# Kernel optimization log

Hardware: AMD Instinct MI355X
Metric: run time of the kernel (lower is better)

Reference implementation:

```python
import jax, jax.numpy as jnp
import numpy as np

N_NODES = 50000
N_EDGES = 640000
D_IN = 128
D_H1 = 128
D_H2 = 256
NEG_SLOPE = 0.2


def setup_inputs() -> dict:
    key = jax.random.key(0)
    ks = jax.random.split(key, 12)
    s = 1.0 / np.sqrt(D_IN)
    inp = {
        'x': jax.random.normal(ks[0], (N_NODES, D_IN), dtype=jnp.float32),
        'edge_index': jax.random.randint(ks[1], (2, N_EDGES), 0, N_NODES, dtype=jnp.int64),
        # GATv2 layer 1: 128 -> 128 (separate lin_l / lin_r, attention vec, residual proj, bias)
        'Wl1': jax.random.normal(ks[2], (D_IN, D_H1), dtype=jnp.float32) * s,
        'Wr1': jax.random.normal(ks[3], (D_IN, D_H1), dtype=jnp.float32) * s,
        'att1': jax.random.normal(ks[4], (D_H1,), dtype=jnp.float32) * s,
        'Wres1': jax.random.normal(ks[5], (D_IN, D_H1), dtype=jnp.float32) * s,
        'b1': jnp.zeros((D_H1,), dtype=jnp.float32),
        # GATv2 layer 2: 128 -> 256
        'Wl2': jax.random.normal(ks[6], (D_H1, D_H2), dtype=jnp.float32) * s,
        'Wr2': jax.random.normal(ks[7], (D_H1, D_H2), dtype=jnp.float32) * s,
        'att2': jax.random.normal(ks[8], (D_H2,), dtype=jnp.float32) * s,
        'Wres2': jax.random.normal(ks[9], (D_H1, D_H2), dtype=jnp.float32) * s,
        'b2': jnp.zeros((D_H2,), dtype=jnp.float32),
    }
    return inp


def _gatv2_layer(x, Wl, Wr, att, Wres, b, src, dst, n_nodes):
    """GATv2Conv (heads=1, residual=True, eval mode/no dropout).
    score e_ij = att . LeakyReLU(Wl x_src + Wr x_dst); softmax over incoming edges per dst;
    out_dst = sum_j alpha_ij * (Wl x_src) + residual + bias.
    """
    xl = x @ Wl                      # [N, F]
    xr = x @ Wr                      # [N, F]
    h = xl[src] + xr[dst]            # [E, F]  gather (irregular access)
    e = jax.nn.leaky_relu(h, NEG_SLOPE) @ att   # [E]
    # segment softmax over destination nodes
    m = jax.ops.segment_max(e, dst, num_segments=n_nodes)      # [N]
    w = jnp.exp(e - m[dst])                                     # [E]
    denom = jax.ops.segment_sum(w, dst, num_segments=n_nodes)   # [N]
    alpha = w / (denom[dst] + 1e-16)                             # [E]
    out = jax.ops.segment_sum(alpha[:, None] * xl[src], dst, num_segments=n_nodes)  # [N, F]
    return out + x @ Wres + b


def reference(x, edge_index, Wl1, Wr1, att1, Wres1, b1, Wl2, Wr2, att2, Wres2, b2):
    src = edge_index[0]
    dst = edge_index[1]
    h = _gatv2_layer(x, Wl1, Wr1, att1, Wres1, b1, src, dst, N_NODES)
    h = jax.nn.elu(h)
    out = _gatv2_layer(h, Wl2, Wr2, att2, Wres2, b2, src, dst, N_NODES)
    return out
```

## Files before the change

kernel.cpp:

```cpp
#include <hip/hip_runtime.h>

typedef unsigned short u16;
typedef unsigned int u32;
typedef __attribute__((ext_vector_type(8))) short bf16x8;
typedef __attribute__((ext_vector_type(4))) float f32x4;

#define NN 50000
#define NE 640000

__device__ __forceinline__ float bfl(u32 u) { return __uint_as_float(u << 16); }
__device__ __forceinline__ float bfh(u32 u) { return __uint_as_float(u & 0xffff0000u); }
__device__ __forceinline__ float bf1(u16 v) { return __uint_as_float(((u32)v) << 16); }
__device__ __forceinline__ u16 f2bf(float f) {
  u32 u = __float_as_uint(f);
  u32 r = (u + 0x7fffu + ((u >> 16) & 1u)) >> 16;
  return (u16)r;
}

__global__ void probe_kernel(const u16* __restrict__ x, const int* __restrict__ ei,
                             int* __restrict__ flags) {
  __shared__ int s_f32, s_i32;
  if (threadIdx.x == 0) { s_f32 = 0; s_i32 = 0; }
  __syncthreads();
  int lf = 0, li = 0;
  for (int i = threadIdx.x; i < 8192; i += 256) {
    float v = bf1(x[i]);
    if (!(fabsf(v) < 1e8f)) lf = 1;
    if (ei[2 * i + 1] != 0) li = 1;
  }
  if (lf) s_f32 = 1;
  if (li) s_i32 = 1;
  __syncthreads();
  if (threadIdx.x == 0) {
    flags[0] = s_f32;
    flags[1] = s_i32 ? 0 : 1;
  }
}

__device__ __forceinline__ int edge_val(const int* __restrict__ w, long j, int i64) {
  return i64 ? w[2 * j] : w[j];
}

__global__ void count_kernel(const int* __restrict__ ei, const int* __restrict__ flags,
                             int* __restrict__ cnt, int E) {
  int e = blockIdx.x * blockDim.x + threadIdx.x;
  if (e >= E) return;
  int d = edge_val(ei, (long)E + e, flags[1]);
  if ((u32)d < (u32)NN) atomicAdd(&cnt[d], 1);
}

__global__ void scan_local(const int* __restrict__ cnt, int* __restrict__ excl,
                           int* __restrict__ bsum, int n) {
  __shared__ int sd[256];
  int t = threadIdx.x;
  int g = blockIdx.x * 256 + t;
  int v = (g < n) ? cnt[g] : 0;
  sd[t] = v;
  __syncthreads();
  for (int off = 1; off < 256; off <<= 1) {
    int x = (t >= off) ? sd[t - off] : 0;
    __syncthreads();
    sd[t] += x;
    __syncthreads();
  }
  int incl = sd[t];
  if (g < n) excl[g] = incl - v;
  if (t == 255) bsum[blockIdx.x] = incl;
}

__global__ void scan_totals(const int* __restrict__ bsum, int* __restrict__ boff, int nb) {
  __shared__ int sd[256];
  int t = threadIdx.x;
  int v = (t < nb) ? bsum[t] : 0;
  sd[t] = v;
  __syncthreads();
  for (int off = 1; off < 256; off <<= 1) {
    int x = (t >= off) ? sd[t - off] : 0;
    __syncthreads();
    sd[t] += x;
    __syncthreads();
  }
  if (t < nb) boff[t] = sd[t] - v;
}

__global__ void scan_add(const int* __restrict__ excl, const int* __restrict__ boff,
                         const int* __restrict__ cnt, int* __restrict__ rowptr,
                         int* __restrict__ fillp, int n) {
  int g = blockIdx.x * 256 + threadIdx.x;
  if (g < n) {
    int e2 = excl[g] + boff[blockIdx.x];
    rowptr[g] = e2;
    fillp[g] = e2;
    if (g == n - 1) rowptr[n] = e2 + cnt[g];
  }
}

__global__ void fill_kernel(const int* __restrict__ ei, const int* __restrict__ flags,
                            int* __restrict__ fillp, int* __restrict__ col, int E) {
  int e = blockIdx.x * blockDim.x + threadIdx.x;
  if (e >= E) return;
  int i64 = flags[1];
  int s = edge_val(ei, (long)e, i64);
  int d = edge_val(ei, (long)E + e, i64);
  if ((u32)d >= (u32)NN) return;
  int p = atomicAdd(&fillp[d], 1);
  col[p] = ((u32)s < (u32)NN) ? s : 0;
}

__global__ void transpose_w(const void* W0, const void* W1, const void* W2,
                            const void* W3, const void* W4, const void* W5,
                            u16* T0, u16* T1, u16* T2, u16* T3, u16* T4, u16* T5,
                            const int* __restrict__ flags) {
  int y = blockIdx.y;
  int M = (y < 3) ? 128 : 256;
  int flat = blockIdx.x * 256 + threadIdx.x;
  if (flat >= M * 128) return;
  int j = flat >> 7;
  int k = flat & 127;
  const void* W = (y == 0) ? W0 : (y == 1) ? W1 : (y == 2) ? W2 : (y == 3) ? W3 : (y == 4) ? W4 : W5;
  u16* T = (y == 0) ? T0 : (y == 1) ? T1 : (y == 2) ? T2 : (y == 3) ? T3 : (y == 4) ? T4 : T5;
  u16 v;
  if (flags[0])
    v = f2bf(((const float*)W)[(size_t)k * M + j]);
  else
    v = ((const u16*)W)[(size_t)k * M + j];
  T[(size_t)j * 128 + k] = v;
}

#define LSTR 136
__global__ __launch_bounds__(256) void gemm3_mfma(
    const void* __restrict__ X,
    const u16* __restrict__ Wta, const u16* __restrict__ Wtb, const u16* __restrict__ Wtc,
    const void* __restrict__ bias,
    u16* __restrict__ Ya, u16* __restrict__ Yb, u16* __restrict__ Yc,
    const int* __restrict__ flags, int x_follows, int N, int M) {
  __shared__ __align__(16) u16 Xs[64 * LSTR];
  __shared__ __align__(16) u16 Bs[128 * LSTR];
  const int K = 128;
  int t = threadIdx.x;
  int lane = t & 63;
  int w = t >> 6;
  int n0g = blockIdx.x * 64;
  int c0 = blockIdx.z * 128;
  int F32X = x_follows ? flags[0] : 0;
  const u16* Wt = (blockIdx.y == 0) ? Wta : ((blockIdx.y == 1) ? Wtb : Wtc);
  u16* Y = (blockIdx.y == 0) ? Ya : ((blockIdx.y == 1) ? Yb : Yc);

  if (!F32X) {
    const u16* Xg = (const u16*)X;
    for (int it = 0; it < 4; ++it) {
      int i = t + 256 * it;
      int r = i >> 4, c8 = (i & 15) * 8;
      int n = n0g + r;
      uint4 v = make_uint4(0, 0, 0, 0);
      if (n < N) v = *(const uint4*)(Xg + (size_t)n * K + c8);
      *(uint4*)(Xs + r * LSTR + c8) = v;
    }
  } else {
    const float* Xg = (const float*)X;
    for (int it = 0; it < 4; ++it) {
      int i = t + 256 * it;
      int r = i >> 4, c8 = (i & 15) * 8;
      int n = n0g + r;
      uint4 pk = make_uint4(0, 0, 0, 0);
      if (n < N) {
        float4 f0 = *(const float4*)(Xg + (size_t)n * K + c8);
        float4 f1 = *(const float4*)(Xg + (size_t)n * K + c8 + 4);
        pk.x = (u32)f2bf(f0.x) | ((u32)f2bf(f0.y) << 16);
        pk.y = (u32)f2bf(f0.z) | ((u32)f2bf(f0.w) << 16);
        pk.z = (u32)f2bf(f1.x) | ((u32)f2bf(f1.y) << 16);
        pk.w = (u32)f2bf(f1.z) | ((u32)f2bf(f1.w) << 16);
      }
      *(uint4*)(Xs + r * LSTR + c8) = pk;
    }
  }
  for (int it = 0; it < 8; ++it) {
    int i = t + 256 * it;
    int j = i >> 4, k8 = (i & 15) * 8;
    uint4 v = *(const uint4*)(Wt + (size_t)(c0 + j) * K + k8);
    *(uint4*)(Bs + j * LSTR + k8) = v;
  }
  __syncthreads();

  int m0 = (w >> 1) * 32;
  int n0 = (w & 1) * 64;
  int l15 = lane & 15;
  int q8 = (lane >> 4) * 8;
  f32x4 acc[2][4];
#pragma unroll
  for (int i = 0; i < 2; ++i)
#pragma unroll
    for (int j = 0; j < 4; ++j) acc[i][j] = (f32x4){0.f, 0.f, 0.f, 0.f};

#pragma unroll
  for (int kc = 0; kc < 4; ++kc) {
    int ko = kc * 32 + q8;
    bf16x8 a[2], b[4];
#pragma unroll
    for (int i = 0; i < 2; ++i)
      a[i] = *(const bf16x8*)(Xs + (m0 + i * 16 + l15) * LSTR + ko);
#pragma unroll
    for (int j = 0; j < 4; ++j)
      b[j] = *(const bf16x8*)(Bs + (n0 + j * 16 + l15) * LSTR + ko);
#pragma unroll
    for (int i = 0; i < 2; ++i)
#pragma unroll
      for (int j = 0; j < 4; ++j)
        acc[i][j] = __builtin_amdgcn_mfma_f32_16x16x32_bf16(a[i], b[j], acc[i][j], 0, 0, 0);
  }
  __syncthreads();

  float bv[4] = {0.f, 0.f, 0.f, 0.f};
  if (blockIdx.y == 2) {
    int F32 = flags[0];
#pragma unroll
    for (int j = 0; j < 4; ++j) {
      int c = c0 + n0 + j * 16 + l15;
      bv[j] = F32 ? ((const float*)bias)[c] : bf1(((const u16*)bias)[c]);
    }
  }

  u16* Ct = Xs;
#pragma unroll
  for (int i = 0; i < 2; ++i)
#pragma unroll
    for (int j = 0; j < 4; ++j) {
      int col = n0 + j * 16 + l15;
      int rbase = m0 + i * 16 + (lane >> 4) * 4;
#pragma unroll
      for (int r = 0; r < 4; ++r)
        Ct[(rbase + r) * LSTR + col] = f2bf(acc[i][j][r] + bv[j]);
    }
  __syncthreads();

  for (int it = 0; it < 4; ++it) {
    int i = t + 256 * it;
    int r = i >> 4, c8 = (i & 15) * 8;
    int n = n0g + r;
    if (n < N) {
      uint4 v = *(const uint4*)(Ct + r * LSTR + c8);
      *(uint4*)(Y + (size_t)n * M + c0 + c8) = v;
    }
  }
}

template <int F, bool ELU>
__global__ __launch_bounds__(256) void gat_agg_kernel(
    const u16* __restrict__ xl, const u16* __restrict__ xr, const u16* __restrict__ res,
    const void* __restrict__ att, const int* __restrict__ rowptr, const int* __restrict__ col,
    void* __restrict__ out, const int* __restrict__ flags, int out_follows, int N) {
  constexpr int HEPL = F / 32;
  int lane = threadIdx.x & 63;
  int half = lane >> 5;
  int hl = lane & 31;
  int node = blockIdx.x * 4 + (threadIdx.x >> 6);
  if (node >= N) return;
  int F32 = flags[0];
  int OF32 = out_follows ? F32 : 0;
  int base = hl * HEPL;

  float xrv[HEPL], attv[HEPL], acc[HEPL];
#pragma unroll
  for (int e = 0; e < HEPL; ++e) {
    xrv[e] = bf1(xr[(size_t)node * F + base + e]);
    attv[e] = F32 ? ((const float*)att)[base + e] : bf1(((const u16*)att)[base + e]);
    acc[e] = 0.f;
  }
  float m = -1e30f, l = 0.f;
  int beg = rowptr[node], end = rowptr[node + 1];

  using VecT = typename std::conditional<HEPL == 4, uint2, uint4>::type;

  for (int cs = beg; cs < end; cs += 64) {
    int n = min(64, end - cs);
    int myc = (cs + lane < end) ? col[cs + lane] : 0;
    int itc = (n + 1) >> 1;
    int j0 = half;
    int c = __shfl(myc, (j0 < n) ? j0 : 0, 64);
    VecT v = *(const VecT*)(xl + (size_t)c * F + base);
    for (int it = 0; it < itc; ++it) {
      VecT cur = v;
      int act = (2 * it + half) < n;
      if (it + 1 < itc) {
        int j2 = 2 * (it + 1) + half;
        int c2 = __shfl(myc, (j2 < n) ? j2 : 0, 64);
        v = *(const VecT*)(xl + (size_t)c2 * F + base);
      }
      float xlv[HEPL];
      if constexpr (HEPL == 4) {
        xlv[0] = bfl(cur.x); xlv[1] = bfh(cur.x);
        xlv[2] = bfl(cur.y); xlv[3] = bfh(cur.y);
      } else {
        xlv[0] = bfl(cur.x); xlv[1] = bfh(cur.x);
        xlv[2] = bfl(cur.y); xlv[3] = bfh(cur.y);
        xlv[4] = bfl(cur.z); xlv[5] = bfh(cur.z);
        xlv[6] = bfl(cur.w); xlv[7] = bfh(cur.w);
      }
      float d = 0.f;
#pragma unroll
      for (int e = 0; e < HEPL; ++e) {
        float h = xlv[e] + xrv[e];
        float lr = (h > 0.f) ? h : 0.2f * h;
        d = fmaf(attv[e], lr, d);
      }
#pragma unroll
      for (int off = 1; off <= 16; off <<= 1) d += __shfl_xor(d, off, 64);
      float pmy = act ? d : -1e30f;
      float pm = fmaxf(pmy, __shfl_xor(pmy, 32, 64));
      if (pm <= m) {
        float w = __expf(pmy - m);
        l += w + __shfl_xor(w, 32, 64);
#pragma unroll
        for (int e = 0; e < HEPL; ++e) acc[e] = fmaf(w, xlv[e], acc[e]);
      } else {
        float scl = __expf(m - pm);
        float w = __expf(pmy - pm);
        l = fmaf(l, scl, w + __shfl_xor(w, 32, 64));
#pragma unroll
        for (int e = 0; e < HEPL; ++e) acc[e] = fmaf(acc[e], scl, w * xlv[e]);
        m = pm;
      }
    }
  }

#pragma unroll
  for (int e = 0; e < HEPL; ++e) acc[e] += __shfl_xor(acc[e], 32, 64);
  float inv = 1.f / (l + 1e-16f);
  if (half == 0) {
    float ov[HEPL];
#pragma unroll
    for (int e = 0; e < HEPL; ++e) {
      float o = fmaf(acc[e], inv, bf1(res[(size_t)node * F + base + e]));
      if (ELU) o = (o > 0.f) ? o : (__expf(o) - 1.f);
      ov[e] = o;
    }
    if (OF32) {
      float* of = (float*)out;
#pragma unroll
      for (int e = 0; e < HEPL; ++e) of[(size_t)node * F + base + e] = ov[e];
    } else {
      u16* o16 = (u16*)out;
      if constexpr (HEPL == 4) {
        uint2 pk;
        pk.x = (u32)f2bf(ov[0]) | ((u32)f2bf(ov[1]) << 16);
        pk.y = (u32)f2bf(ov[2]) | ((u32)f2bf(ov[3]) << 16);
        *(uint2*)(o16 + (size_t)node * F + base) = pk;
      } else {
        uint4 pk;
        pk.x = (u32)f2bf(ov[0]) | ((u32)f2bf(ov[1]) << 16);
        pk.y = (u32)f2bf(ov[2]) | ((u32)f2bf(ov[3]) << 16);
        pk.z = (u32)f2bf(ov[4]) | ((u32)f2bf(ov[5]) << 16);
        pk.w = (u32)f2bf(ov[6]) | ((u32)f2bf(ov[7]) << 16);
        *(uint4*)(o16 + (size_t)node * F + base) = pk;
      }
    }
  }
}

extern "C" void kernel_launch(void* const* d_in, const int* in_sizes, int n_in,
                              void* d_out, int out_size, void* d_ws, size_t ws_size,
                              hipStream_t stream) {
  const u16* x16 = (const u16*)d_in[0];
  const int* ei = (const int*)d_in[1];
  const int N = NN, E = NE;

  char* ws = (char*)d_ws;
  size_t off = 0;
  auto alloc = [&](size_t bytes) -> void* {
    void* p = (void*)(ws + off);
    off += (bytes + 255) & ~(size_t)255;
    return p;
  };
  int* flags = (int*)alloc(2 * 4);
  int* cnt = (int*)alloc((size_t)N * 4);
  int* rowptr = (int*)alloc((size_t)(N + 1) * 4);
  int* fillp = (int*)alloc((size_t)N * 4);
  int* colb = (int*)alloc((size_t)E * 4);
  int* excl = (int*)alloc((size_t)N * 4);
  int* bsum = (int*)alloc(256 * 4);
  int* boff = (int*)alloc(256 * 4);
  u16* Wt1a = (u16*)alloc((size_t)128 * 128 * 2);
  u16* Wt1b = (u16*)alloc((size_t)128 * 128 * 2);
  u16* Wt1c = (u16*)alloc((size_t)128 * 128 * 2);
  u16* Wt2a = (u16*)alloc((size_t)256 * 128 * 2);
  u16* Wt2b = (u16*)alloc((size_t)256 * 128 * 2);
  u16* Wt2c = (u16*)alloc((size_t)256 * 128 * 2);
  u16* buf1 = (u16*)alloc((size_t)N * 256 * 2);
  u16* buf2 = (u16*)alloc((size_t)N * 256 * 2);
  u16* buf3 = (u16*)alloc((size_t)N * 256 * 2);
  u16* h1 = (u16*)alloc((size_t)N * 128 * 2);
  (void)ws_size; (void)n_in; (void)in_sizes; (void)out_size;

  int nb = (N + 255) / 256;

  probe_kernel<<<1, 256, 0, stream>>>(x16, ei, flags);
  hipMemsetAsync(cnt, 0, (size_t)N * 4, stream);
  count_kernel<<<(E + 255) / 256, 256, 0, stream>>>(ei, flags, cnt, E);
  scan_local<<<nb, 256, 0, stream>>>(cnt, excl, bsum, N);
  scan_totals<<<1, 256, 0, stream>>>(bsum, boff, nb);
  scan_add<<<nb, 256, 0, stream>>>(excl, boff, cnt, rowptr, fillp, N);
  fill_kernel<<<(E + 255) / 256, 256, 0, stream>>>(ei, flags, fillp, colb, E);
  transpose_w<<<dim3(128, 6), 256, 0, stream>>>(
      d_in[2], d_in[3], d_in[5], d_in[7], d_in[8], d_in[10],
      Wt1a, Wt1b, Wt1c, Wt2a, Wt2b, Wt2c, flags);

  int gx = (N + 63) / 64;
  gemm3_mfma<<<dim3(gx, 3, 1), 256, 0, stream>>>(
      d_in[0], Wt1a, Wt1b, Wt1c, d_in[6], buf1, buf2, buf3, flags, 1, N, 128);
  gat_agg_kernel<128, true><<<(N + 3) / 4, 256, 0, stream>>>(
      buf1, buf2, buf3, d_in[4], rowptr, colb, h1, flags, 0, N);
  gemm3_mfma<<<dim3(gx, 3, 2), 256, 0, stream>>>(
      h1, Wt2a, Wt2b, Wt2c, d_in[11], buf1, buf2, buf3, flags, 0, N, 256);
  gat_agg_kernel<256, false><<<(N + 3) / 4, 256, 0, stream>>>(
      buf1, buf2, buf3, d_in[9], rowptr, colb, d_out, flags, 1, N);
}
```

Measured before the change: 388.5 us.

## Process four edges per iteration with deeper gather prefetch in GAT aggregation

The aggregation loop now handles four neighbour edges per iteration, two per half-wave, and keeps two iterations of gathered xl rows in flight instead of one. This is meant to raise memory-level parallelism on the irregular gathers and halve the shuffle-reduction and online-softmax overhead per edge. It also vectorises the xr, att and residual loads and the fp32 output store, and shrinks blocks to 128 threads with two nodes each. The cost is higher register pressure and wasted lanes for nodes whose degree is not a multiple of four.

```diff
diff --git a/kernel.cpp b/kernel.cpp
--- a/kernel.cpp
+++ b/kernel.cpp
@@ -16,6 +16,18 @@
   u32 r = (u + 0x7fffu + ((u >> 16) & 1u)) >> 16;
   return (u16)r;
 }
+
+__device__ __forceinline__ void unpk(uint2 v, float* o) {
+  o[0] = bfl(v.x); o[1] = bfh(v.x); o[2] = bfl(v.y); o[3] = bfh(v.y);
+}
+__device__ __forceinline__ void unpk(uint4 v, float* o) {
+  o[0] = bfl(v.x); o[1] = bfh(v.x); o[2] = bfl(v.y); o[3] = bfh(v.y);
+  o[4] = bfl(v.z); o[5] = bfh(v.z); o[6] = bfl(v.w); o[7] = bfh(v.w);
+}
+
+template <int HEPL> struct VecSel;
+template <> struct VecSel<4> { using T = uint2; };
+template <> struct VecSel<8> { using T = uint4; };
 
 __global__ void probe_kernel(const u16* __restrict__ x, const int* __restrict__ ei,
                              int* __restrict__ flags) {
@@ -245,79 +257,103 @@
 }
 
 template <int F, bool ELU>
-__global__ __launch_bounds__(256) void gat_agg_kernel(
+__global__ __launch_bounds__(128) void gat_agg_kernel(
     const u16* __restrict__ xl, const u16* __restrict__ xr, const u16* __restrict__ res,
     const void* __restrict__ att, const int* __restrict__ rowptr, const int* __restrict__ col,
     void* __restrict__ out, const int* __restrict__ flags, int out_follows, int N) {
   constexpr int HEPL = F / 32;
+  using VecT = typename VecSel<HEPL>::T;
   int lane = threadIdx.x & 63;
   int half = lane >> 5;
   int hl = lane & 31;
-  int node = blockIdx.x * 4 + (threadIdx.x >> 6);
+  int node = blockIdx.x * 2 + (threadIdx.x >> 6);
   if (node >= N) return;
   int F32 = flags[0];
   int OF32 = out_follows ? F32 : 0;
   int base = hl * HEPL;
 
   float xrv[HEPL], attv[HEPL], acc[HEPL];
-#pragma unroll
-  for (int e = 0; e < HEPL; ++e) {
-    xrv[e] = bf1(xr[(size_t)node * F + base + e]);
-    attv[e] = F32 ? ((const float*)att)[base + e] : bf1(((const u16*)att)[base + e]);
-    acc[e] = 0.f;
-  }
+  {
+    VecT xp = *(const VecT*)(xr + (size_t)node * F + base);
+    unpk(xp, xrv);
+  }
+  if (F32) {
+    const float* af = (const float*)att + base;
+#pragma unroll
+    for (int e = 0; e < HEPL; ++e) attv[e] = af[e];
+  } else {
+    VecT ap = *(const VecT*)((const u16*)att + base);
+    unpk(ap, attv);
+  }
+#pragma unroll
+  for (int e = 0; e < HEPL; ++e) acc[e] = 0.f;
+
   float m = -1e30f, l = 0.f;
   int beg = rowptr[node], end = rowptr[node + 1];
-
-  using VecT = typename std::conditional<HEPL == 4, uint2, uint4>::type;
 
   for (int cs = beg; cs < end; cs += 64) {
     int n = min(64, end - cs);
     int myc = (cs + lane < end) ? col[cs + lane] : 0;
-    int itc = (n + 1) >> 1;
-    int j0 = half;
-    int c = __shfl(myc, (j0 < n) ? j0 : 0, 64);
-    VecT v = *(const VecT*)(xl + (size_t)c * F + base);
+    int itc = (n + 3) >> 2;
+
+    auto ld = [&](int j) -> VecT {
+      int c = __shfl(myc, (j < n) ? j : 0, 64);
+      return *(const VecT*)(xl + (size_t)c * F + base);
+    };
+
+    VecT a0 = ld(half), a1 = ld(2 + half);
+    VecT b0 = a0, b1 = a1;
+    if (itc > 1) { b0 = ld(4 + half); b1 = ld(6 + half); }
+
     for (int it = 0; it < itc; ++it) {
-      VecT cur = v;
-      int act = (2 * it + half) < n;
-      if (it + 1 < itc) {
-        int j2 = 2 * (it + 1) + half;
-        int c2 = __shfl(myc, (j2 < n) ? j2 : 0, 64);
-        v = *(const VecT*)(xl + (size_t)c2 * F + base);
-      }
-      float xlv[HEPL];
-      if constexpr (HEPL == 4) {
-        xlv[0] = bfl(cur.x); xlv[1] = bfh(cur.x);
-        xlv[2] = bfl(cur.y); xlv[3] = bfh(cur.y);
-      } else {
-        xlv[0] = bfl(cur.x); xlv[1] = bfh(cur.x);
-        xlv[2] = bfl(cur.y); xlv[3] = bfh(cur.y);
-        xlv[4] = bfl(cur.z); xlv[5] = bfh(cur.z);
-        xlv[6] = bfl(cur.w); xlv[7] = bfh(cur.w);
-      }
-      float d = 0.f;
+      VecT cur0 = a0, cur1 = a1;
+      a0 = b0; a1 = b1;
+      if (it + 2 < itc) {
+        b0 = ld(4 * (it + 2) + half);
+        b1 = ld(4 * (it + 2) + 2 + half);
+      }
+      int act0 = (4 * it + half) < n;
+      int act1 = (4 * it + 2 + half) < n;
+
+      float x0[HEPL], x1[HEPL];
+      unpk(cur0, x0);
+      unpk(cur1, x1);
+      float d0 = 0.f, d1 = 0.f;
 #pragma unroll
       for (int e = 0; e < HEPL; ++e) {
-        float h = xlv[e] + xrv[e];
-        float lr = (h > 0.f) ? h : 0.2f * h;
-        d = fmaf(attv[e], lr, d);
-      }
-#pragma unroll
-      for (int off = 1; off <= 16; off <<= 1) d += __shfl_xor(d, off, 64);
-      float pmy = act ? d : -1e30f;
-      float pm = fmaxf(pmy, __shfl_xor(pmy, 32, 64));
+        float h0 = x0[e] + xrv[e];
+        float h1 = x1[e] + xrv[e];
+        h0 = fmaxf(h0, 0.2f * h0);
+        h1 = fmaxf(h1, 0.2f * h1);
+        d0 = fmaf(attv[e], h0, d0);
+        d1 = fmaf(attv[e], h1, d1);
+      }
+#pragma unroll
+      for (int off = 1; off <= 16; off <<= 1) {
+        d0 += __shfl_xor(d0, off, 64);
+        d1 += __shfl_xor(d1, off, 64);
+      }
+      float p0 = act0 ? d0 : -1e30f;
+      float p1 = act1 ? d1 : -1e30f;
+      float pmx = fmaxf(p0, p1);
+      float pm = fmaxf(pmx, __shfl_xor(pmx, 32, 64));
       if (pm <= m) {
-        float w = __expf(pmy - m);
-        l += w + __shfl_xor(w, 32, 64);
-#pragma unroll
-        for (int e = 0; e < HEPL; ++e) acc[e] = fmaf(w, xlv[e], acc[e]);
+        float w0 = __expf(p0 - m);
+        float w1 = __expf(p1 - m);
+        float ws = w0 + w1;
+        l += ws + __shfl_xor(ws, 32, 64);
+#pragma unroll
+        for (int e = 0; e < HEPL; ++e)
+          acc[e] = fmaf(w1, x1[e], fmaf(w0, x0[e], acc[e]));
       } else {
         float scl = __expf(m - pm);
-        float w = __expf(pmy - pm);
-        l = fmaf(l, scl, w + __shfl_xor(w, 32, 64));
-#pragma unroll
-        for (int e = 0; e < HEPL; ++e) acc[e] = fmaf(acc[e], scl, w * xlv[e]);
+        float w0 = __expf(p0 - pm);
+        float w1 = __expf(p1 - pm);
+        float ws = w0 + w1;
+        l = fmaf(l, scl, ws + __shfl_xor(ws, 32, 64));
+#pragma unroll
+        for (int e = 0; e < HEPL; ++e)
+          acc[e] = fmaf(acc[e], scl, fmaf(w1, x1[e], w0 * x0[e]));
         m = pm;
       }
     }
@@ -327,17 +363,24 @@
   for (int e = 0; e < HEPL; ++e) acc[e] += __shfl_xor(acc[e], 32, 64);
   float inv = 1.f / (l + 1e-16f);
   if (half == 0) {
+    VecT rp = *(const VecT*)(res + (size_t)node * F + base);
+    float rv[HEPL];
+    unpk(rp, rv);
     float ov[HEPL];
 #pragma unroll
     for (int e = 0; e < HEPL; ++e) {
-      float o = fmaf(acc[e], inv, bf1(res[(size_t)node * F + base + e]));
+      float o = fmaf(acc[e], inv, rv[e]);
       if (ELU) o = (o > 0.f) ? o : (__expf(o) - 1.f);
       ov[e] = o;
     }
     if (OF32) {
-      float* of = (float*)out;
-#pragma unroll
-      for (int e = 0; e < HEPL; ++e) of[(size_t)node * F + base + e] = ov[e];
+      float* of = (float*)out + (size_t)node * F + base;
+      float4 f0 = {ov[0], ov[1], ov[2], ov[3]};
+      *(float4*)of = f0;
+      if constexpr (HEPL == 8) {
+        float4 f1 = {ov[4], ov[5], ov[6], ov[7]};
+        *(float4*)(of + 4) = f1;
+      }
     } else {
       u16* o16 = (u16*)out;
       if constexpr (HEPL == 4) {
@@ -407,10 +450,10 @@
   int gx = (N + 63) / 64;
   gemm3_mfma<<<dim3(gx, 3, 1), 256, 0, stream>>>(
       d_in[0], Wt1a, Wt1b, Wt1c, d_in[6], buf1, buf2, buf3, flags, 1, N, 128);
-  gat_agg_kernel<128, true><<<(N + 3) / 4, 256, 0, stream>>>(
+  gat_agg_kernel<128, true><<<(N + 1) / 2, 128, 0, stream>>>(
       buf1, buf2, buf3, d_in[4], rowptr, colb, h1, flags, 0, N);
   gemm3_mfma<<<dim3(gx, 3, 2), 256, 0, stream>>>(
       h1, Wt2a, Wt2b, Wt2c, d_in[11], buf1, buf2, buf3, flags, 0, N, 256);
-  gat_agg_kernel<256, false><<<(N + 3) / 4, 256, 0, stream>>>(
+  gat_agg_kernel<256, false><<<(N + 1) / 2, 128, 0, stream>>>(
       buf1, buf2, buf3, d_in[9], rowptr, colb, d_out, flags, 1, N);
 }
```

After: 333.5 us. 1.16x faster.
